# Performance work log

Measured on AMD Instinct MI355X. Metric: run time of the kernel, lower is better.

The kernel has to match this reference:

```python
import jax, jax.numpy as jnp
import numpy as np

# PyTorch LSTM gate order: i, f, g, o. Dropout layers are identity in eval mode.

def _lstm_step(w_ih, w_hh, b):
    def step(carry, xt):
        h, c = carry
        g = xt @ w_ih.T + h @ w_hh.T + b
        i, f, gg, o = jnp.split(g, 4, axis=-1)
        c = jax.nn.sigmoid(f) * c + jax.nn.sigmoid(i) * jnp.tanh(gg)
        h = jax.nn.sigmoid(o) * jnp.tanh(c)
        return (h, c), h
    return step


def bilstm(x, wf_ih, wf_hh, bf_ih, bf_hh, wb_ih, wb_hh, bb_ih, bb_hh):
    # x: [B, T, D] -> out: [B, T, 2H]
    B = x.shape[0]
    H = wf_hh.shape[1]
    xt = jnp.swapaxes(x, 0, 1)  # [T, B, D]
    init = (jnp.zeros((B, H), x.dtype), jnp.zeros((B, H), x.dtype))
    _, hf = jax.lax.scan(_lstm_step(wf_ih, wf_hh, bf_ih + bf_hh), init, xt)
    _, hb = jax.lax.scan(_lstm_step(wb_ih, wb_hh, bb_ih + bb_hh), init, xt[::-1])
    hb = hb[::-1]
    return jnp.swapaxes(jnp.concatenate([hf, hb], axis=-1), 0, 1)


def setup_inputs() -> dict:
    key = jax.random.key(0)
    ks = iter(jax.random.split(key, 64))
    d = {"x": jax.random.normal(next(ks), (1024, 1024, 8), jnp.float32)}
    layer_dims = [(16, 20), (40, 20), (40, 10), (20, 10)]
    for li, (din, H) in enumerate(layer_dims, start=1):
        for dr in ("f", "b"):
            d[f"w{li}{dr}_ih"] = 0.1 * jax.random.normal(next(ks), (4 * H, din), jnp.float32)
            d[f"w{li}{dr}_hh"] = 0.1 * jax.random.normal(next(ks), (4 * H, H), jnp.float32)
            d[f"b{li}{dr}_ih"] = 0.1 * jax.random.normal(next(ks), (4 * H,), jnp.float32)
            d[f"b{li}{dr}_hh"] = 0.1 * jax.random.normal(next(ks), (4 * H,), jnp.float32)
    d["fc_w"] = 0.1 * jax.random.normal(next(ks), (1, 20), jnp.float32)
    d["fc_b"] = 0.1 * jax.random.normal(next(ks), (1,), jnp.float32)
    return d


def reference(x,
              w1f_ih, w1f_hh, b1f_ih, b1f_hh, w1b_ih, w1b_hh, b1b_ih, b1b_hh,
              w2f_ih, w2f_hh, b2f_ih, b2f_hh, w2b_ih, w2b_hh, b2b_ih, b2b_hh,
              w3f_ih, w3f_hh, b3f_ih, b3f_hh, w3b_ih, w3b_hh, b3b_ih, b3b_hh,
              w4f_ih, w4f_hh, b4f_ih, b4f_hh, w4b_ih, w4b_hh, b4b_ih, b4b_hh,
              fc_w, fc_b):
    # lag-1 concat: [B,T,8] -> [B,T,16]
    x_lag = jnp.concatenate([jnp.zeros_like(x[:, :1, :]), x[:, :-1, :]], axis=1)
    h = jnp.concatenate([x, x_lag], axis=2)
    h = bilstm(h, w1f_ih, w1f_hh, b1f_ih, b1f_hh, w1b_ih, w1b_hh, b1b_ih, b1b_hh)
    h = bilstm(h, w2f_ih, w2f_hh, b2f_ih, b2f_hh, w2b_ih, w2b_hh, b2b_ih, b2b_hh)
    h = bilstm(h, w3f_ih, w3f_hh, b3f_ih, b3f_hh, w3b_ih, w3b_hh, b3b_ih, b3b_hh)
    h = bilstm(h, w4f_ih, w4f_hh, b4f_ih, b4f_hh, w4b_ih, w4b_hh, b4b_ih, b4b_hh)
    h = h[:, -1, :]  # [B, 20]
    return jax.nn.sigmoid(h @ fc_w.T + fc_b)
```

## Files before the change

kernel.cpp:

```cpp
#include <hip/hip_runtime.h>
#include <hip/hip_fp16.h>
#include <stdint.h>

#define B_TOTAL 1024
#define T_TOTAL 1024
#define LOG2E 1.44269504088896f

typedef _Float16 f16x2 __attribute__((ext_vector_type(2)));

__device__ __forceinline__ float dot2acc(uint32_t xw, f16x2 w, float acc) {
#if __has_builtin(__builtin_amdgcn_fdot2)
    return __builtin_amdgcn_fdot2(__builtin_bit_cast(f16x2, xw), w, acc, false);
#else
    f16x2 xv = __builtin_bit_cast(f16x2, xw);
    return acc + (float)xv.x * (float)w.x + (float)xv.y * (float)w.y;
#endif
}

__device__ __forceinline__ uint32_t packf2(float a, float b) {
    f16x2 t;
    t.x = (_Float16)a;
    t.y = (_Float16)b;
    return __builtin_bit_cast(uint32_t, t);
}

__device__ __forceinline__ float sigm_(float z) {
    float e = __builtin_amdgcn_exp2f(-LOG2E * z);
    return __builtin_amdgcn_rcpf(1.0f + e);
}
__device__ __forceinline__ float tanh_(float z) {
    float e = __builtin_amdgcn_exp2f((2.0f * LOG2E) * z);
    float r = __builtin_amdgcn_rcpf(1.0f + e);
    return __builtin_fmaf(-2.0f, r, 1.0f);
}

__device__ __forceinline__ void wavebar() {
#if __has_builtin(__builtin_amdgcn_wave_barrier)
    __builtin_amdgcn_wave_barrier();
#endif
}

template <int DIN, int H, bool LAYER1, bool STORE_ALL>
__global__ void __launch_bounds__(64, 1) lstm_scan(
    const float* __restrict__ x,
    const __half* __restrict__ inbuf,
    const float* __restrict__ wihf, const float* __restrict__ whhf,
    const float* __restrict__ bihf, const float* __restrict__ bhhf,
    const float* __restrict__ wihb, const float* __restrict__ whhb,
    const float* __restrict__ bihb, const float* __restrict__ bhhb,
    __half* __restrict__ outbuf,
    float* __restrict__ lasth)
{
    constexpr int GPW   = 64 / H;
    constexpr int ND    = DIN / 2;
    constexpr int NH    = H / 2;
    constexpr int HS_DW = (H == 20) ? 12 : 8;

    const int dir  = blockIdx.y;
    const int lane = threadIdx.x;
    const int g    = lane / H;
    const int j    = lane - g * H;
    const int b    = blockIdx.x * GPW + g;
    const bool valid = (g < GPW) && (b < B_TOTAL);
    const int bs   = valid ? b : (B_TOTAL - 1);

    const float* w_ih = dir ? wihb : wihf;
    const float* w_hh = dir ? whhb : whhf;
    const float* b_ih = dir ? bihb : bihf;
    const float* b_hh = dir ? bhhb : bhhf;

    __shared__ uint32_t hsm[GPW + 1][HS_DW];

    f16x2 wih2[4][ND];
    f16x2 whh2[4][NH];
    float bias[4];
#pragma unroll
    for (int q = 0; q < 4; ++q) {
        const int r = q * H + j;
#pragma unroll
        for (int d = 0; d < ND; ++d) {
            f16x2 t;
            t.x = (_Float16)w_ih[r * DIN + 2 * d];
            t.y = (_Float16)w_ih[r * DIN + 2 * d + 1];
            wih2[q][d] = t;
        }
#pragma unroll
        for (int k = 0; k < NH; ++k) {
            f16x2 t;
            t.x = (_Float16)w_hh[r * H + 2 * k];
            t.y = (_Float16)w_hh[r * H + 2 * k + 1];
            whh2[q][k] = t;
        }
        bias[q] = b_ih[r] + b_hh[r];
    }

    const int tstep = dir ? -1 : 1;
    int tt = dir ? (T_TOTAL - 1) : 0;

    __half* op = nullptr;
    ptrdiff_t opstep = 0;
    if constexpr (STORE_ALL) {
        op = outbuf + (size_t)tt * (B_TOTAL * 2 * H) + (size_t)bs * (2 * H) + dir * H + j;
        opstep = (ptrdiff_t)tstep * (B_TOTAL * 2 * H);
    }

    float c = 0.0f;
    float hlast = 0.0f;
    ((__half*)&hsm[g][0])[j] = __float2half(0.0f);
    wavebar();

    auto tail = [&](const uint32_t* hd, float a0, float a1, float a2, float a3) {
#pragma unroll
        for (int k = 0; k < NH; ++k) {
            a0 = dot2acc(hd[k], whh2[0][k], a0);
            a1 = dot2acc(hd[k], whh2[1][k], a1);
            a2 = dot2acc(hd[k], whh2[2][k], a2);
            a3 = dot2acc(hd[k], whh2[3][k], a3);
        }
        const float iv = sigm_(a0);
        const float fv = sigm_(a1);
        const float gv = tanh_(a2);
        const float ov = sigm_(a3);
        c = __builtin_fmaf(fv, c, iv * gv);
        const float h = ov * tanh_(c);
        ((__half*)&hsm[g][0])[j] = __float2half(h);
        wavebar();
        if constexpr (STORE_ALL) {
            if (valid) *op = __float2half(h);
            op += opstep;
        } else {
            hlast = h;
        }
        tt += tstep;
    };

    if constexpr (LAYER1) {
        const float* xrow = x + (size_t)bs * (T_TOTAL * 8);
        uint32_t xcur[4], xlag[4];
        {
            const float4* p = (const float4*)(xrow + (size_t)tt * 8);
            float4 u0 = p[0], u1 = p[1];
            xcur[0] = packf2(u0.x, u0.y); xcur[1] = packf2(u0.z, u0.w);
            xcur[2] = packf2(u1.x, u1.y); xcur[3] = packf2(u1.z, u1.w);
            if (dir) {
                const float4* q = (const float4*)(xrow + (size_t)(tt - 1) * 8);
                float4 v0 = q[0], v1 = q[1];
                xlag[0] = packf2(v0.x, v0.y); xlag[1] = packf2(v0.z, v0.w);
                xlag[2] = packf2(v1.x, v1.y); xlag[3] = packf2(v1.z, v1.w);
            } else {
#pragma unroll
                for (int d = 0; d < 4; ++d) xlag[d] = 0u;
            }
        }

        for (int t = 0; t < T_TOTAL; ++t) {
            uint32_t hd[NH];
#pragma unroll
            for (int k = 0; k < NH; ++k) hd[k] = hsm[g][k];

            float a0 = bias[0], a1 = bias[1], a2 = bias[2], a3 = bias[3];
#pragma unroll
            for (int d = 0; d < 4; ++d) {
                a0 = dot2acc(xcur[d], wih2[0][d], a0);
                a1 = dot2acc(xcur[d], wih2[1][d], a1);
                a2 = dot2acc(xcur[d], wih2[2][d], a2);
                a3 = dot2acc(xcur[d], wih2[3][d], a3);
            }
#pragma unroll
            for (int d = 0; d < 4; ++d) {
                a0 = dot2acc(xlag[d], wih2[0][4 + d], a0);
                a1 = dot2acc(xlag[d], wih2[1][4 + d], a1);
                a2 = dot2acc(xlag[d], wih2[2][4 + d], a2);
                a3 = dot2acc(xlag[d], wih2[3][4 + d], a3);
            }

            const int li = dir ? (tt - 2) : (tt + 1);
            const bool ld = (li >= 0) && (li < T_TOTAL);
            float4 n0 = {0, 0, 0, 0}, n1 = {0, 0, 0, 0};
            if (ld) {
                const float4* p = (const float4*)(xrow + (size_t)li * 8);
                n0 = p[0];
                n1 = p[1];
            }

            tail(hd, a0, a1, a2, a3);

            uint32_t np[4] = {packf2(n0.x, n0.y), packf2(n0.z, n0.w),
                              packf2(n1.x, n1.y), packf2(n1.z, n1.w)};
            if (dir == 0) {
#pragma unroll
                for (int d = 0; d < 4; ++d) { xlag[d] = xcur[d]; xcur[d] = np[d]; }
            } else {
#pragma unroll
                for (int d = 0; d < 4; ++d) {
                    xcur[d] = xlag[d];
                    xlag[d] = ld ? np[d] : 0u;
                }
            }
        }
    } else {
        const ptrdiff_t ipstep = (ptrdiff_t)tstep * (B_TOTAL * ND);
        const uint32_t* ip = (const uint32_t*)inbuf + (size_t)tt * (B_TOTAL * ND) + (size_t)bs * ND;

        uint32_t xb[4][ND];
#pragma unroll
        for (int s = 0; s < 3; ++s) {
#pragma unroll
            for (int d = 0; d < ND; ++d) xb[s][d] = ip[d];
            ip += ipstep;
        }

        auto step = [&](const uint32_t* xc, uint32_t* xn, bool pf) {
            uint32_t hd[NH];
#pragma unroll
            for (int k = 0; k < NH; ++k) hd[k] = hsm[g][k];

            float a0 = bias[0], a1 = bias[1], a2 = bias[2], a3 = bias[3];
#pragma unroll
            for (int d = 0; d < ND; ++d) {
                a0 = dot2acc(xc[d], wih2[0][d], a0);
                a1 = dot2acc(xc[d], wih2[1][d], a1);
                a2 = dot2acc(xc[d], wih2[2][d], a2);
                a3 = dot2acc(xc[d], wih2[3][d], a3);
            }
            if (pf) {
#pragma unroll
                for (int d = 0; d < ND; ++d) xn[d] = ip[d];
                ip += ipstep;
            }
            tail(hd, a0, a1, a2, a3);
        };

        for (int t = 0; t < T_TOTAL; t += 4) {
            step(xb[0], xb[3], t + 3 < T_TOTAL);
            step(xb[1], xb[0], t + 4 < T_TOTAL);
            step(xb[2], xb[1], t + 5 < T_TOTAL);
            step(xb[3], xb[2], t + 6 < T_TOTAL);
        }
    }

    if constexpr (!STORE_ALL) {
        if (valid) lasth[b * H + j] = hlast;
    }
}

__global__ void final_kernel(const __half* __restrict__ l3out,
                             const float* __restrict__ hf4,
                             const float* __restrict__ w_ih,
                             const float* __restrict__ b_ih,
                             const float* __restrict__ b_hh,
                             const float* __restrict__ fc_w,
                             const float* __restrict__ fc_b,
                             float* __restrict__ out)
{
    const int b = blockIdx.x * blockDim.x + threadIdx.x;
    if (b >= B_TOTAL) return;

    float in4[20];
    const __half* p = l3out + (size_t)(T_TOTAL - 1) * (B_TOTAL * 20) + (size_t)b * 20;
#pragma unroll
    for (int i = 0; i < 20; ++i) in4[i] = __half2float(p[i]);

    float z = fc_b[0];
#pragma unroll
    for (int k = 0; k < 10; ++k) z += fc_w[k] * hf4[b * 10 + k];

#pragma unroll
    for (int k = 0; k < 10; ++k) {
        float gi = b_ih[k]      + b_hh[k];
        float gg = b_ih[20 + k] + b_hh[20 + k];
        float go = b_ih[30 + k] + b_hh[30 + k];
#pragma unroll
        for (int i = 0; i < 20; ++i) {
            const float xi = in4[i];
            gi += w_ih[k * 20 + i]        * xi;
            gg += w_ih[(20 + k) * 20 + i] * xi;
            go += w_ih[(30 + k) * 20 + i] * xi;
        }
        const float cc = sigm_(gi) * tanh_(gg);
        const float hb = sigm_(go) * tanh_(cc);
        z += fc_w[10 + k] * hb;
    }
    out[b] = sigm_(z);
}

extern "C" void kernel_launch(void* const* d_in, const int* in_sizes, int n_in,
                              void* d_out, int out_size, void* d_ws, size_t ws_size,
                              hipStream_t stream) {
    const float* x = (const float*)d_in[0];
    auto W = [&](int li, int dr, int k) -> const float* {
        return (const float*)d_in[1 + (li - 1) * 8 + dr * 4 + k];
    };
    const float* fc_w = (const float*)d_in[33];
    const float* fc_b = (const float*)d_in[34];
    float* out = (float*)d_out;

    __half* buf0 = (__half*)d_ws;
    __half* buf1 = buf0 + (size_t)T_TOTAL * B_TOTAL * 40;
    float* hf4 = (float*)(buf1 + (size_t)T_TOTAL * B_TOTAL * 40);

    lstm_scan<16, 20, true, true><<<dim3(342, 2, 1), 64, 0, stream>>>(
        x, nullptr,
        W(1,0,0), W(1,0,1), W(1,0,2), W(1,0,3),
        W(1,1,0), W(1,1,1), W(1,1,2), W(1,1,3),
        buf0, nullptr);

    lstm_scan<40, 20, false, true><<<dim3(342, 2, 1), 64, 0, stream>>>(
        nullptr, buf0,
        W(2,0,0), W(2,0,1), W(2,0,2), W(2,0,3),
        W(2,1,0), W(2,1,1), W(2,1,2), W(2,1,3),
        buf1, nullptr);

    lstm_scan<40, 10, false, true><<<dim3(171, 2, 1), 64, 0, stream>>>(
        nullptr, buf1,
        W(3,0,0), W(3,0,1), W(3,0,2), W(3,0,3),
        W(3,1,0), W(3,1,1), W(3,1,2), W(3,1,3),
        buf0, nullptr);

    lstm_scan<20, 10, false, false><<<dim3(171, 1, 1), 64, 0, stream>>>(
        nullptr, buf0,
        W(4,0,0), W(4,0,1), W(4,0,2), W(4,0,3),
        W(4,0,0), W(4,0,1), W(4,0,2), W(4,0,3),
        nullptr, hf4);

    final_kernel<<<dim3(4, 1, 1), 256, 0, stream>>>(
        buf0, hf4, W(4,1,0), W(4,1,2), W(4,1,3), fc_w, fc_b, out);
}
```

Before: 1.737 ms.

## Split LSTM scan into producer and consumer waves via shared-memory ring

Each block now runs two waves. A producer wave computes the input projection (x·W_ih + bias) ahead of time and writes it into a 16-slot shared-memory ring with per-slot flags. A consumer wave spins on those flags, then runs only the recurrent h·W_hh product and the gate nonlinearities. The aim is to take the input-projection work and the global loads off the serial recurrence's critical path. The cost is twice the threads per block, volatile LDS polling and spin-wait overhead, and correctness that depends on the ordering of plain volatile shared-memory accesses without fences.

```diff
diff --git a/kernel.cpp b/kernel.cpp
--- a/kernel.cpp
+++ b/kernel.cpp
@@ -41,7 +41,8 @@
 }
 
 template <int DIN, int H, bool LAYER1, bool STORE_ALL>
-__global__ void __launch_bounds__(64, 1) lstm_scan(
+__global__ void __launch_bounds__(128)
+__attribute__((amdgpu_waves_per_eu(2))) lstm_pc(
     const float* __restrict__ x,
     const __half* __restrict__ inbuf,
     const float* __restrict__ wihf, const float* __restrict__ whhf,
@@ -54,193 +55,236 @@
     constexpr int GPW   = 64 / H;
     constexpr int ND    = DIN / 2;
     constexpr int NH    = H / 2;
+    constexpr int SLOTS = 16;
     constexpr int HS_DW = (H == 20) ? 12 : 8;
 
     const int dir  = blockIdx.y;
     const int lane = threadIdx.x;
+    const int wv   = threadIdx.y;
     const int g    = lane / H;
     const int j    = lane - g * H;
     const int b    = blockIdx.x * GPW + g;
     const bool valid = (g < GPW) && (b < B_TOTAL);
     const int bs   = valid ? b : (B_TOTAL - 1);
 
-    const float* w_ih = dir ? wihb : wihf;
-    const float* w_hh = dir ? whhb : whhf;
-    const float* b_ih = dir ? bihb : bihf;
-    const float* b_hh = dir ? bhhb : bhhf;
-
+    __shared__ float    gxs[SLOTS][4][64];
+    __shared__ int      flags[SLOTS];
+    __shared__ int      consprog;
     __shared__ uint32_t hsm[GPW + 1][HS_DW];
 
-    f16x2 wih2[4][ND];
-    f16x2 whh2[4][NH];
-    float bias[4];
-#pragma unroll
-    for (int q = 0; q < 4; ++q) {
-        const int r = q * H + j;
-#pragma unroll
-        for (int d = 0; d < ND; ++d) {
-            f16x2 t;
-            t.x = (_Float16)w_ih[r * DIN + 2 * d];
-            t.y = (_Float16)w_ih[r * DIN + 2 * d + 1];
-            wih2[q][d] = t;
-        }
-#pragma unroll
-        for (int k = 0; k < NH; ++k) {
-            f16x2 t;
-            t.x = (_Float16)w_hh[r * H + 2 * k];
-            t.y = (_Float16)w_hh[r * H + 2 * k + 1];
-            whh2[q][k] = t;
-        }
-        bias[q] = b_ih[r] + b_hh[r];
+    volatile float* vgx   = (volatile float*)&gxs[0][0][0];
+    volatile int*   vflg  = flags;
+    volatile int*   vcons = &consprog;
+
+    if (wv == 0) {
+        if (lane < SLOTS) flags[lane] = 0;
+        if (lane == 0) consprog = -1;
+        ((__half*)&hsm[g][0])[j] = __float2half(0.0f);
     }
+    __syncthreads();
 
     const int tstep = dir ? -1 : 1;
     int tt = dir ? (T_TOTAL - 1) : 0;
 
-    __half* op = nullptr;
-    ptrdiff_t opstep = 0;
-    if constexpr (STORE_ALL) {
-        op = outbuf + (size_t)tt * (B_TOTAL * 2 * H) + (size_t)bs * (2 * H) + dir * H + j;
-        opstep = (ptrdiff_t)tstep * (B_TOTAL * 2 * H);
-    }
-
-    float c = 0.0f;
-    float hlast = 0.0f;
-    ((__half*)&hsm[g][0])[j] = __float2half(0.0f);
-    wavebar();
-
-    auto tail = [&](const uint32_t* hd, float a0, float a1, float a2, float a3) {
-#pragma unroll
-        for (int k = 0; k < NH; ++k) {
-            a0 = dot2acc(hd[k], whh2[0][k], a0);
-            a1 = dot2acc(hd[k], whh2[1][k], a1);
-            a2 = dot2acc(hd[k], whh2[2][k], a2);
-            a3 = dot2acc(hd[k], whh2[3][k], a3);
-        }
-        const float iv = sigm_(a0);
-        const float fv = sigm_(a1);
-        const float gv = tanh_(a2);
-        const float ov = sigm_(a3);
-        c = __builtin_fmaf(fv, c, iv * gv);
-        const float h = ov * tanh_(c);
-        ((__half*)&hsm[g][0])[j] = __float2half(h);
-        wavebar();
+    if (wv == 1) {
+        const float* w_ih = dir ? wihb : wihf;
+        const float* b_i  = dir ? bihb : bihf;
+        const float* b_h  = dir ? bhhb : bhhf;
+
+        f16x2 wih2[4][ND];
+        float bias[4];
+#pragma unroll
+        for (int q = 0; q < 4; ++q) {
+            const int r = q * H + j;
+#pragma unroll
+            for (int d = 0; d < ND; ++d) {
+                f16x2 t;
+                t.x = (_Float16)w_ih[r * DIN + 2 * d];
+                t.y = (_Float16)w_ih[r * DIN + 2 * d + 1];
+                wih2[q][d] = t;
+            }
+            bias[q] = b_i[r] + b_h[r];
+        }
+
+        auto emit = [&](int s, float a0, float a1, float a2, float a3) {
+            if (s >= SLOTS) {
+                while (*vcons < s - SLOTS) __builtin_amdgcn_s_sleep(1);
+            }
+            const int slot = s & (SLOTS - 1);
+            volatile float* p = vgx + slot * (4 * 64) + lane;
+            p[0]   = a0;
+            p[64]  = a1;
+            p[128] = a2;
+            p[192] = a3;
+            vflg[slot] = s + 1;
+        };
+
+        if constexpr (LAYER1) {
+            const float* xrow = x + (size_t)bs * (T_TOTAL * 8);
+            uint32_t xcur[4], xlag[4];
+            {
+                const float4* pp = (const float4*)(xrow + (size_t)tt * 8);
+                float4 u0 = pp[0], u1 = pp[1];
+                xcur[0] = packf2(u0.x, u0.y); xcur[1] = packf2(u0.z, u0.w);
+                xcur[2] = packf2(u1.x, u1.y); xcur[3] = packf2(u1.z, u1.w);
+                if (dir) {
+                    const float4* qq = (const float4*)(xrow + (size_t)(tt - 1) * 8);
+                    float4 v0 = qq[0], v1 = qq[1];
+                    xlag[0] = packf2(v0.x, v0.y); xlag[1] = packf2(v0.z, v0.w);
+                    xlag[2] = packf2(v1.x, v1.y); xlag[3] = packf2(v1.z, v1.w);
+                } else {
+#pragma unroll
+                    for (int d = 0; d < 4; ++d) xlag[d] = 0u;
+                }
+            }
+
+            for (int s = 0; s < T_TOTAL; ++s) {
+                float a0 = bias[0], a1 = bias[1], a2 = bias[2], a3 = bias[3];
+#pragma unroll
+                for (int d = 0; d < 4; ++d) {
+                    a0 = dot2acc(xcur[d], wih2[0][d], a0);
+                    a1 = dot2acc(xcur[d], wih2[1][d], a1);
+                    a2 = dot2acc(xcur[d], wih2[2][d], a2);
+                    a3 = dot2acc(xcur[d], wih2[3][d], a3);
+                }
+#pragma unroll
+                for (int d = 0; d < 4; ++d) {
+                    a0 = dot2acc(xlag[d], wih2[0][4 + d], a0);
+                    a1 = dot2acc(xlag[d], wih2[1][4 + d], a1);
+                    a2 = dot2acc(xlag[d], wih2[2][4 + d], a2);
+                    a3 = dot2acc(xlag[d], wih2[3][4 + d], a3);
+                }
+
+                const int li = dir ? (tt - 2) : (tt + 1);
+                const bool ld = (li >= 0) && (li < T_TOTAL);
+                float4 n0 = {0, 0, 0, 0}, n1 = {0, 0, 0, 0};
+                if (ld) {
+                    const float4* pp = (const float4*)(xrow + (size_t)li * 8);
+                    n0 = pp[0];
+                    n1 = pp[1];
+                }
+
+                emit(s, a0, a1, a2, a3);
+
+                uint32_t np[4] = {packf2(n0.x, n0.y), packf2(n0.z, n0.w),
+                                  packf2(n1.x, n1.y), packf2(n1.z, n1.w)};
+                if (dir == 0) {
+#pragma unroll
+                    for (int d = 0; d < 4; ++d) { xlag[d] = xcur[d]; xcur[d] = np[d]; }
+                } else {
+#pragma unroll
+                    for (int d = 0; d < 4; ++d) {
+                        xcur[d] = xlag[d];
+                        xlag[d] = ld ? np[d] : 0u;
+                    }
+                }
+                tt += tstep;
+            }
+        } else {
+            const ptrdiff_t ipstep = (ptrdiff_t)tstep * (B_TOTAL * ND);
+            const uint32_t* ip = (const uint32_t*)inbuf + (size_t)tt * (B_TOTAL * ND) + (size_t)bs * ND;
+
+            uint32_t xq0[ND], xq1[ND];
+#pragma unroll
+            for (int d = 0; d < ND; ++d) xq0[d] = ip[d];
+            ip += ipstep;
+#pragma unroll
+            for (int d = 0; d < ND; ++d) xq1[d] = ip[d];
+            ip += ipstep;
+
+            auto pstep = [&](const uint32_t* xc, uint32_t* xn, int s, bool pf) {
+                float a0 = bias[0], a1 = bias[1], a2 = bias[2], a3 = bias[3];
+#pragma unroll
+                for (int d = 0; d < ND; ++d) {
+                    a0 = dot2acc(xc[d], wih2[0][d], a0);
+                    a1 = dot2acc(xc[d], wih2[1][d], a1);
+                    a2 = dot2acc(xc[d], wih2[2][d], a2);
+                    a3 = dot2acc(xc[d], wih2[3][d], a3);
+                }
+                if (pf) {
+#pragma unroll
+                    for (int d = 0; d < ND; ++d) xn[d] = ip[d];
+                    ip += ipstep;
+                }
+                emit(s, a0, a1, a2, a3);
+            };
+
+            for (int s = 0; s < T_TOTAL; s += 2) {
+                pstep(xq0, xq0, s, s + 2 < T_TOTAL);
+                pstep(xq1, xq1, s + 1, s + 3 < T_TOTAL);
+            }
+        }
+    } else {
+        const float* w_hh = dir ? whhb : whhf;
+        f16x2 whh2[4][NH];
+#pragma unroll
+        for (int q = 0; q < 4; ++q) {
+            const int r = q * H + j;
+#pragma unroll
+            for (int k = 0; k < NH; ++k) {
+                f16x2 t;
+                t.x = (_Float16)w_hh[r * H + 2 * k];
+                t.y = (_Float16)w_hh[r * H + 2 * k + 1];
+                whh2[q][k] = t;
+            }
+        }
+
+        __half* op = nullptr;
+        ptrdiff_t opstep = 0;
         if constexpr (STORE_ALL) {
-            if (valid) *op = __float2half(h);
-            op += opstep;
-        } else {
-            hlast = h;
-        }
-        tt += tstep;
-    };
-
-    if constexpr (LAYER1) {
-        const float* xrow = x + (size_t)bs * (T_TOTAL * 8);
-        uint32_t xcur[4], xlag[4];
-        {
-            const float4* p = (const float4*)(xrow + (size_t)tt * 8);
-            float4 u0 = p[0], u1 = p[1];
-            xcur[0] = packf2(u0.x, u0.y); xcur[1] = packf2(u0.z, u0.w);
-            xcur[2] = packf2(u1.x, u1.y); xcur[3] = packf2(u1.z, u1.w);
-            if (dir) {
-                const float4* q = (const float4*)(xrow + (size_t)(tt - 1) * 8);
-                float4 v0 = q[0], v1 = q[1];
-                xlag[0] = packf2(v0.x, v0.y); xlag[1] = packf2(v0.z, v0.w);
-                xlag[2] = packf2(v1.x, v1.y); xlag[3] = packf2(v1.z, v1.w);
+            op = outbuf + (size_t)tt * (B_TOTAL * 2 * H) + (size_t)bs * (2 * H) + dir * H + j;
+            opstep = (ptrdiff_t)tstep * (B_TOTAL * 2 * H);
+        }
+
+        float c = 0.0f;
+        float hlast = 0.0f;
+
+        for (int s = 0; s < T_TOTAL; ++s) {
+            const int slot = s & (SLOTS - 1);
+            const int want = s + 1;
+            volatile float* p = vgx + slot * (4 * 64) + lane;
+            float a0, a1, a2, a3;
+            int fl;
+            do {
+                fl = vflg[slot];
+                a0 = p[0];
+                a1 = p[64];
+                a2 = p[128];
+                a3 = p[192];
+            } while (fl != want);
+            if ((s & 3) == 3) {
+                if (lane == 0) *vcons = s;
+            }
+
+            uint32_t hd[NH];
+#pragma unroll
+            for (int k = 0; k < NH; ++k) hd[k] = hsm[g][k];
+#pragma unroll
+            for (int k = 0; k < NH; ++k) {
+                a0 = dot2acc(hd[k], whh2[0][k], a0);
+                a1 = dot2acc(hd[k], whh2[1][k], a1);
+                a2 = dot2acc(hd[k], whh2[2][k], a2);
+                a3 = dot2acc(hd[k], whh2[3][k], a3);
+            }
+            const float iv = sigm_(a0);
+            const float fv = sigm_(a1);
+            const float gv = tanh_(a2);
+            const float ov = sigm_(a3);
+            c = __builtin_fmaf(fv, c, iv * gv);
+            const float h = ov * tanh_(c);
+            ((__half*)&hsm[g][0])[j] = __float2half(h);
+            wavebar();
+            if constexpr (STORE_ALL) {
+                if (valid) *op = __float2half(h);
+                op += opstep;
             } else {
-#pragma unroll
-                for (int d = 0; d < 4; ++d) xlag[d] = 0u;
-            }
-        }
-
-        for (int t = 0; t < T_TOTAL; ++t) {
-            uint32_t hd[NH];
-#pragma unroll
-            for (int k = 0; k < NH; ++k) hd[k] = hsm[g][k];
-
-            float a0 = bias[0], a1 = bias[1], a2 = bias[2], a3 = bias[3];
-#pragma unroll
-            for (int d = 0; d < 4; ++d) {
-                a0 = dot2acc(xcur[d], wih2[0][d], a0);
-                a1 = dot2acc(xcur[d], wih2[1][d], a1);
-                a2 = dot2acc(xcur[d], wih2[2][d], a2);
-                a3 = dot2acc(xcur[d], wih2[3][d], a3);
-            }
-#pragma unroll
-            for (int d = 0; d < 4; ++d) {
-                a0 = dot2acc(xlag[d], wih2[0][4 + d], a0);
-                a1 = dot2acc(xlag[d], wih2[1][4 + d], a1);
-                a2 = dot2acc(xlag[d], wih2[2][4 + d], a2);
-                a3 = dot2acc(xlag[d], wih2[3][4 + d], a3);
-            }
-
-            const int li = dir ? (tt - 2) : (tt + 1);
-            const bool ld = (li >= 0) && (li < T_TOTAL);
-            float4 n0 = {0, 0, 0, 0}, n1 = {0, 0, 0, 0};
-            if (ld) {
-                const float4* p = (const float4*)(xrow + (size_t)li * 8);
-                n0 = p[0];
-                n1 = p[1];
-            }
-
-            tail(hd, a0, a1, a2, a3);
-
-            uint32_t np[4] = {packf2(n0.x, n0.y), packf2(n0.z, n0.w),
-                              packf2(n1.x, n1.y), packf2(n1.z, n1.w)};
-            if (dir == 0) {
-#pragma unroll
-                for (int d = 0; d < 4; ++d) { xlag[d] = xcur[d]; xcur[d] = np[d]; }
-            } else {
-#pragma unroll
-                for (int d = 0; d < 4; ++d) {
-                    xcur[d] = xlag[d];
-                    xlag[d] = ld ? np[d] : 0u;
-                }
-            }
-        }
-    } else {
-        const ptrdiff_t ipstep = (ptrdiff_t)tstep * (B_TOTAL * ND);
-        const uint32_t* ip = (const uint32_t*)inbuf + (size_t)tt * (B_TOTAL * ND) + (size_t)bs * ND;
-
-        uint32_t xb[4][ND];
-#pragma unroll
-        for (int s = 0; s < 3; ++s) {
-#pragma unroll
-            for (int d = 0; d < ND; ++d) xb[s][d] = ip[d];
-            ip += ipstep;
-        }
-
-        auto step = [&](const uint32_t* xc, uint32_t* xn, bool pf) {
-            uint32_t hd[NH];
-#pragma unroll
-            for (int k = 0; k < NH; ++k) hd[k] = hsm[g][k];
-
-            float a0 = bias[0], a1 = bias[1], a2 = bias[2], a3 = bias[3];
-#pragma unroll
-            for (int d = 0; d < ND; ++d) {
-                a0 = dot2acc(xc[d], wih2[0][d], a0);
-                a1 = dot2acc(xc[d], wih2[1][d], a1);
-                a2 = dot2acc(xc[d], wih2[2][d], a2);
-                a3 = dot2acc(xc[d], wih2[3][d], a3);
-            }
-            if (pf) {
-#pragma unroll
-                for (int d = 0; d < ND; ++d) xn[d] = ip[d];
-                ip += ipstep;
-            }
-            tail(hd, a0, a1, a2, a3);
-        };
-
-        for (int t = 0; t < T_TOTAL; t += 4) {
-            step(xb[0], xb[3], t + 3 < T_TOTAL);
-            step(xb[1], xb[0], t + 4 < T_TOTAL);
-            step(xb[2], xb[1], t + 5 < T_TOTAL);
-            step(xb[3], xb[2], t + 6 < T_TOTAL);
-        }
-    }
-
-    if constexpr (!STORE_ALL) {
-        if (valid) lasth[b * H + j] = hlast;
+                hlast = h;
+            }
+        }
+
+        if constexpr (!STORE_ALL) {
+            if (valid) lasth[b * H + j] = hlast;
+        }
     }
 }
 
@@ -299,25 +343,25 @@
     __half* buf1 = buf0 + (size_t)T_TOTAL * B_TOTAL * 40;
     float* hf4 = (float*)(buf1 + (size_t)T_TOTAL * B_TOTAL * 40);
 
-    lstm_scan<16, 20, true, true><<<dim3(342, 2, 1), 64, 0, stream>>>(
+    lstm_pc<16, 20, true, true><<<dim3(342, 2, 1), dim3(64, 2, 1), 0, stream>>>(
         x, nullptr,
         W(1,0,0), W(1,0,1), W(1,0,2), W(1,0,3),
         W(1,1,0), W(1,1,1), W(1,1,2), W(1,1,3),
         buf0, nullptr);
 
-    lstm_scan<40, 20, false, true><<<dim3(342, 2, 1), 64, 0, stream>>>(
+    lstm_pc<40, 20, false, true><<<dim3(342, 2, 1), dim3(64, 2, 1), 0, stream>>>(
         nullptr, buf0,
         W(2,0,0), W(2,0,1), W(2,0,2), W(2,0,3),
         W(2,1,0), W(2,1,1), W(2,1,2), W(2,1,3),
         buf1, nullptr);
 
-    lstm_scan<40, 10, false, true><<<dim3(171, 2, 1), 64, 0, stream>>>(
+    lstm_pc<40, 10, false, true><<<dim3(171, 2, 1), dim3(64, 2, 1), 0, stream>>>(
         nullptr, buf1,
         W(3,0,0), W(3,0,1), W(3,0,2), W(3,0,3),
         W(3,1,0), W(3,1,1), W(3,1,2), W(3,1,3),
         buf0, nullptr);
 
-    lstm_scan<20, 10, false, false><<<dim3(171, 1, 1), 64, 0, stream>>>(
+    lstm_pc<20, 10, false, false><<<dim3(171, 1, 1), dim3(64, 2, 1), 0, stream>>>(
         nullptr, buf0,
         W(4,0,0), W(4,0,1), W(4,0,2), W(4,0,3),
         W(4,0,0), W(4,0,1), W(4,0,2), W(4,0,3),
```

Measured after the change: 2.656 ms. +52.9%, slower.
